# Optimization experiments

Hardware: AMD Instinct MI355X
Metric: run time of the kernel (lower is better)

The kernel has to match this reference:

```python
import jax, jax.numpy as jnp
import numpy as np

NUM_NODES = 19
INPUT_DIM = 100
HIDDEN = 128
SEQ_LEN = 250
BATCH = 64
NUM_CLASSES = 4


def setup_inputs() -> dict:
    key = jax.random.key(0)
    ks = jax.random.split(key, 12)
    s_in = 1.0 / np.sqrt(HIDDEN)  # PyTorch LSTM init scale
    inputs = jax.random.normal(ks[0], (BATCH, NUM_NODES, SEQ_LEN, INPUT_DIM), dtype=jnp.float32)
    seq_lengths = jax.random.randint(ks[1], (BATCH,), 1, SEQ_LEN + 1, dtype=jnp.int64)
    # Per-node LSTM weights, PyTorch gate order (i, f, g, o) stacked on first axis.
    W_ih = jax.random.uniform(ks[2], (NUM_NODES, 4 * HIDDEN, INPUT_DIM), jnp.float32, -s_in, s_in)
    W_hh = jax.random.uniform(ks[3], (NUM_NODES, 4 * HIDDEN, HIDDEN), jnp.float32, -s_in, s_in)
    b_ih = jax.random.uniform(ks[4], (NUM_NODES, 4 * HIDDEN), jnp.float32, -s_in, s_in)
    b_hh = jax.random.uniform(ks[5], (NUM_NODES, 4 * HIDDEN), jnp.float32, -s_in, s_in)
    feat = NUM_NODES * HIDDEN
    s1 = 1.0 / np.sqrt(feat)
    s2 = 1.0 / np.sqrt(128)
    W1 = jax.random.uniform(ks[6], (128, feat), jnp.float32, -s1, s1)
    b1 = jax.random.uniform(ks[7], (128,), jnp.float32, -s1, s1)
    W2 = jax.random.uniform(ks[8], (NUM_CLASSES, 128), jnp.float32, -s2, s2)
    b2 = jax.random.uniform(ks[9], (NUM_CLASSES,), jnp.float32, -s2, s2)
    return {"inputs": inputs, "seq_lengths": seq_lengths,
            "W_ih": W_ih, "W_hh": W_hh, "b_ih": b_ih, "b_hh": b_hh,
            "W1": W1, "b1": b1, "W2": W2, "b2": b2}


def _grouped_lstm_last(inputs, W_ih, W_hh, b_ih, b_hh):
    # inputs: [B, N, T, D] -> last hidden state per node, [B, N, H]
    B, N, T, D = inputs.shape
    H = W_hh.shape[-1]
    x = jnp.transpose(inputs, (2, 1, 0, 3))  # [T, N, B, D]
    # Precompute input projections for all timesteps: [T, N, B, 4H]
    xg = jnp.einsum('tnbd,ngd->tnbg', x, W_ih) + (b_ih + b_hh)[None, :, None, :]

    def step(carry, xg_t):
        h, c = carry  # [N, B, H]
        gates = xg_t + jnp.einsum('nbh,ngh->nbg', h, W_hh)  # [N, B, 4H]
        i, f, g, o = jnp.split(gates, 4, axis=-1)  # PyTorch gate order i,f,g,o
        i = jax.nn.sigmoid(i)
        f = jax.nn.sigmoid(f)
        g = jnp.tanh(g)
        o = jax.nn.sigmoid(o)
        c = f * c + i * g
        h = o * jnp.tanh(c)
        return (h, c), None

    h0 = jnp.zeros((N, B, H), dtype=inputs.dtype)
    (h_last, _), _ = jax.lax.scan(step, (h0, h0), xg)
    return jnp.transpose(h_last, (1, 0, 2))  # [B, N, H]


def reference(inputs, seq_lengths, W_ih, W_hh, b_ih, b_hh, W1, b1, W2, b2):
    h = _grouped_lstm_last(inputs, W_ih, W_hh, b_ih, b_hh)  # [B, N, H]
    combined = h.reshape(h.shape[0], -1)  # concat over nodes -> [B, N*H]
    hidden = jax.nn.relu(combined @ W1.T + b1)  # dropout inactive (eval)
    return hidden @ W2.T + b2  # [B, num_classes]
```

## Files before the change

### kernel.cpp

```cpp
#include <hip/hip_runtime.h>
#include <hip/hip_bf16.h>

#define NN   19
#define DIN  100
#define HID  128
#define TT   250
#define BB   64
#define NC   4
#define FEAT 2432

typedef __attribute__((ext_vector_type(8))) short s8v;
typedef __attribute__((ext_vector_type(4))) float f4v;
typedef _Float16 h8v __attribute__((ext_vector_type(8)));
typedef _Float16 h4v __attribute__((ext_vector_type(4)));

#define BFI_USH   1245184
#define V2_OFF_BFI  0ull
#define V2_OFF_BFH  2490368ull
#define V2_OFF_BIAS 4980736ull
#define V2_OFF_W1T  5019648ull
#define V2_OFF_HF   6264832ull
#define V2_NEED     6887424ull
#define PACK2_TOTAL (2*BFI_USH + 19*512 + FEAT*HID)

#define SZ_BF   (NN*8*4*8*512)
#define OFF_W1T_O (SZ_BF/2)
#define SZ_W1T  (FEAT*HID)
#define OFF_HF_O  (OFF_W1T_O + SZ_W1T)
#define PACK_TOTAL_O (SZ_BF + SZ_W1T)

__device__ __forceinline__ unsigned short f2bf(float x) {
    union { float f; unsigned u; } v; v.f = x;
    unsigned r = v.u + 0x7FFF + ((v.u >> 16) & 1);
    return (unsigned short)(r >> 16);
}
#define LOG2E 1.4426950408889634f
__device__ __forceinline__ float sigf(float x) {
    return __builtin_amdgcn_rcpf(1.f + __builtin_amdgcn_exp2f(-LOG2E * x));
}
__device__ __forceinline__ float tnhf(float x) {
    return 1.f - 2.f * __builtin_amdgcn_rcpf(__builtin_amdgcn_exp2f(2.f * LOG2E * x) + 1.f);
}

__device__ __forceinline__ void lgkm_barrier() {
    asm volatile("s_waitcnt lgkmcnt(0)" ::: "memory");
    __builtin_amdgcn_s_barrier();
    asm volatile("" ::: "memory");
}


__global__ __launch_bounds__(256) void pack2_kernel(
        const float* __restrict__ W_ih, const float* __restrict__ W_hh,
        const float* __restrict__ b_ih, const float* __restrict__ b_hh,
        const float* __restrict__ W1, char* __restrict__ wsb) {
    int id = blockIdx.x * 256 + threadIdx.x;
    if (id < 2 * BFI_USH) {
        int which = id >= BFI_USH;
        int i = which ? id - BFI_USH : id;
        int e    = i & 7;
        int lane = (i >> 3) & 63;
        int kt   = (i >> 9) & 3;
        int nt   = (i >> 11) & 3;
        int hb   = (i >> 13) & 7;
        int n    = i >> 16;
        int k = kt * 32 + (lane >> 4) * 8 + e;
        int g = nt * 128 + hb * 16 + (lane & 15);
        float v;
        if (which) v = W_hh[((size_t)n * 512 + g) * HID + k];
        else       v = (k < DIN) ? W_ih[((size_t)n * 512 + g) * DIN + k] : 0.f;
        reinterpret_cast<_Float16*>(wsb)[id] = (_Float16)v;
        return;
    }
    int id2 = id - 2 * BFI_USH;
    if (id2 < NN * 512) {
        reinterpret_cast<float*>(wsb + V2_OFF_BIAS)[id2] = b_ih[id2] + b_hh[id2];
        return;
    }
    int id3 = id2 - NN * 512;
    if (id3 < FEAT * HID) {
        int j = id3 & 127, k = id3 >> 7;
        reinterpret_cast<float*>(wsb + V2_OFF_W1T)[id3] = W1[(size_t)j * FEAT + k];
    }
}

__global__ __launch_bounds__(512, 2) void lstm8_kernel(
        const char* __restrict__ wsb, const float* __restrict__ inp,
        float* __restrict__ hf) {
    __shared__ alignas(16) _Float16 wih[8 * 16 * 512];
    __shared__ alignas(16) _Float16 xh[2][16 * 256];

    const int tid  = threadIdx.x;
    const int lane = tid & 63;
    const int w8   = tid >> 6;
    const int l15  = lane & 15;
    const int g4   = lane >> 4;
    const int n    = blockIdx.x >> 3;
    const int oct  = blockIdx.x & 7;
    const int bq   = oct >> 1;
    const int hi   = oct & 1;
    const int hb   = w8;
    const int j    = hb * 16 + l15;

    h8v bf[4][4];
    {
        const _Float16* wp = reinterpret_cast<const _Float16*>(wsb + V2_OFF_BFH)
                             + (size_t)lane * 8;
        #pragma unroll
        for (int nt = 0; nt < 4; ++nt)
            #pragma unroll
            for (int kt = 0; kt < 4; ++kt)
                bf[nt][kt] = *reinterpret_cast<const h8v*>(
                    wp + ((size_t)((n * 8 + hb) * 16 + nt * 4 + kt)) * 512);
    }
    float bs[4];
    #pragma unroll
    for (int nt = 0; nt < 4; ++nt)
        bs[nt] = reinterpret_cast<const float*>(wsb + V2_OFF_BIAS)[n * 512 + nt * 128 + j];

    {
        const h8v* src = reinterpret_cast<const h8v*>(
            reinterpret_cast<const _Float16*>(wsb + V2_OFF_BFI) + (size_t)n * 65536);
        h8v* dst = reinterpret_cast<h8v*>(wih);
        for (int i = tid; i < 8192; i += 512) dst[i] = src[i];
    }
    for (int i = tid; i < 2 * 16 * 256; i += 512) (&xh[0][0])[i] = (_Float16)0.f;

    const bool st = tid < 200;
    const int sr  = st ? tid / 25 : 0;
    const int c4  = st ? tid - sr * 25 : 0;
    const int g4s = sr >> 1, qs = sr & 1;
    const int tr  = g4s * 4 + qs;
    const int Rr  = (g4s & 1) * 4 + (g4s >> 1) * 2 + qs;
    const float* xb = inp + (size_t)((bq * 16 + hi * 8 + Rr) * NN + n) * (TT * DIN)
                      + c4 * 4;
    const int wofs_x = tr * 512 + ((c4 * 8) ^ ((tr & 7) << 4));

    const int arow = l15 * 512;
    const int aswz = (l15 & 7) << 4;
    const int wr0 = (g4 * 4) * 512 + ((256 + 2 * j) ^ (((g4 * 4) & 7) << 4));
    const int wr1 = (g4 * 4 + 1) * 512 + ((256 + 2 * j) ^ (((g4 * 4 + 1) & 7) << 4));
    const char* wfb = reinterpret_cast<const char*>(wih) + hb * 16384 + lane * 16;

    float c2[2] = {0.f, 0.f};
    float h2[2] = {0.f, 0.f};

    __syncthreads();
    if (st) {
        float4 v = *reinterpret_cast<const float4*>(xb);
        h4v pk = {(_Float16)v.x, (_Float16)v.y, (_Float16)v.z, (_Float16)v.w};
        *reinterpret_cast<h4v*>(reinterpret_cast<char*>(xh[0]) + wofs_x) = pk;
    }
    __syncthreads();

    #pragma unroll 2
    for (int t = 0; t < TT; ++t) {
        char* rc = reinterpret_cast<char*>(xh[t & 1]);
        char* wc = reinterpret_cast<char*>(xh[(t + 1) & 1]);

        float4 nxt = make_float4(0.f, 0.f, 0.f, 0.f);
        if (t < TT - 1 && st)
            nxt = *reinterpret_cast<const float4*>(xb + (t + 1) * DIN);

        f4v acc[4];
        #pragma unroll
        for (int nt = 0; nt < 4; ++nt)
            acc[nt] = (f4v){bs[nt], bs[nt], 0.f, 0.f};

        h8v ax0 = *reinterpret_cast<const h8v*>(rc + arow + ((0 * 64 + g4 * 16) ^ aswz));
        h8v ax1 = *reinterpret_cast<const h8v*>(rc + arow + ((1 * 64 + g4 * 16) ^ aswz));
        h8v ax2 = *reinterpret_cast<const h8v*>(rc + arow + ((2 * 64 + g4 * 16) ^ aswz));
        h8v ax3 = *reinterpret_cast<const h8v*>(rc + arow + ((3 * 64 + g4 * 16) ^ aswz));
        #pragma unroll
        for (int nt = 0; nt < 4; ++nt) {
            h8v w0 = *reinterpret_cast<const h8v*>(wfb + (nt * 4 + 0) * 1024);
            h8v w1 = *reinterpret_cast<const h8v*>(wfb + (nt * 4 + 1) * 1024);
            h8v w2 = *reinterpret_cast<const h8v*>(wfb + (nt * 4 + 2) * 1024);
            h8v w3 = *reinterpret_cast<const h8v*>(wfb + (nt * 4 + 3) * 1024);
            acc[nt] = __builtin_amdgcn_mfma_f32_16x16x32_f16(ax0, w0, acc[nt], 0, 0, 0);
            acc[nt] = __builtin_amdgcn_mfma_f32_16x16x32_f16(ax1, w1, acc[nt], 0, 0, 0);
            acc[nt] = __builtin_amdgcn_mfma_f32_16x16x32_f16(ax2, w2, acc[nt], 0, 0, 0);
            acc[nt] = __builtin_amdgcn_mfma_f32_16x16x32_f16(ax3, w3, acc[nt], 0, 0, 0);
        }

        h8v ah0 = *reinterpret_cast<const h8v*>(rc + arow + ((4 * 64 + g4 * 16) ^ aswz));
        h8v ah1 = *reinterpret_cast<const h8v*>(rc + arow + ((5 * 64 + g4 * 16) ^ aswz));
        h8v ah2 = *reinterpret_cast<const h8v*>(rc + arow + ((6 * 64 + g4 * 16) ^ aswz));
        h8v ah3 = *reinterpret_cast<const h8v*>(rc + arow + ((7 * 64 + g4 * 16) ^ aswz));

        acc[0] = __builtin_amdgcn_mfma_f32_16x16x32_f16(ah0, bf[0][0], acc[0], 0, 0, 0);
        acc[0] = __builtin_amdgcn_mfma_f32_16x16x32_f16(ah1, bf[0][1], acc[0], 0, 0, 0);
        acc[0] = __builtin_amdgcn_mfma_f32_16x16x32_f16(ah2, bf[0][2], acc[0], 0, 0, 0);
        acc[0] = __builtin_amdgcn_mfma_f32_16x16x32_f16(ah3, bf[0][3], acc[0], 0, 0, 0);
        float ii0 = sigf(acc[0][0]);
        float ii1 = sigf(acc[0][1]);

        acc[1] = __builtin_amdgcn_mfma_f32_16x16x32_f16(ah0, bf[1][0], acc[1], 0, 0, 0);
        acc[1] = __builtin_amdgcn_mfma_f32_16x16x32_f16(ah1, bf[1][1], acc[1], 0, 0, 0);
        acc[1] = __builtin_amdgcn_mfma_f32_16x16x32_f16(ah2, bf[1][2], acc[1], 0, 0, 0);
        acc[1] = __builtin_amdgcn_mfma_f32_16x16x32_f16(ah3, bf[1][3], acc[1], 0, 0, 0);
        float ff0 = sigf(acc[1][0]);
        float ff1 = sigf(acc[1][1]);

        acc[2] = __builtin_amdgcn_mfma_f32_16x16x32_f16(ah0, bf[2][0], acc[2], 0, 0, 0);
        acc[2] = __builtin_amdgcn_mfma_f32_16x16x32_f16(ah1, bf[2][1], acc[2], 0, 0, 0);
        acc[2] = __builtin_amdgcn_mfma_f32_16x16x32_f16(ah2, bf[2][2], acc[2], 0, 0, 0);
        acc[2] = __builtin_amdgcn_mfma_f32_16x16x32_f16(ah3, bf[2][3], acc[2], 0, 0, 0);
        float gg0 = tnhf(acc[2][0]);
        float gg1 = tnhf(acc[2][1]);

        acc[3] = __builtin_amdgcn_mfma_f32_16x16x32_f16(ah0, bf[3][0], acc[3], 0, 0, 0);
        acc[3] = __builtin_amdgcn_mfma_f32_16x16x32_f16(ah1, bf[3][1], acc[3], 0, 0, 0);
        acc[3] = __builtin_amdgcn_mfma_f32_16x16x32_f16(ah2, bf[3][2], acc[3], 0, 0, 0);
        acc[3] = __builtin_amdgcn_mfma_f32_16x16x32_f16(ah3, bf[3][3], acc[3], 0, 0, 0);
        float oo0 = sigf(acc[3][0]);
        float oo1 = sigf(acc[3][1]);

        float cn0 = ff0 * c2[0] + ii0 * gg0;
        c2[0] = cn0;
        float hn0 = oo0 * tnhf(cn0);
        h2[0] = hn0;
        *reinterpret_cast<_Float16*>(wc + wr0) = (_Float16)hn0;

        float cn1 = ff1 * c2[1] + ii1 * gg1;
        c2[1] = cn1;
        float hn1 = oo1 * tnhf(cn1);
        h2[1] = hn1;
        *reinterpret_cast<_Float16*>(wc + wr1) = (_Float16)hn1;

        if (t < TT - 1 && st) {
            h4v pk = {(_Float16)nxt.x, (_Float16)nxt.y, (_Float16)nxt.z, (_Float16)nxt.w};
            *reinterpret_cast<h4v*>(wc + wofs_x) = pk;
        }
        lgkm_barrier();
    }

    #pragma unroll
    for (int q = 0; q < 2; ++q) {
        int b = bq * 16 + hi * 8 + (g4 & 1) * 4 + (g4 >> 1) * 2 + q;
        hf[((size_t)b * NN + n) * HID + j] = h2[q];
    }
}

__global__ __launch_bounds__(256) void head2_kernel(
        const float* __restrict__ hf, const float* __restrict__ w1t,
        const float* __restrict__ b1, const float* __restrict__ W2,
        const float* __restrict__ b2, float* __restrict__ out) {
    __shared__ float comb[FEAT];
    __shared__ float par[2][HID];
    __shared__ float hid[HID];
    const int b = blockIdx.x;
    const int u  = threadIdx.x & 127;
    const int kk = threadIdx.x >> 7;
    const float* hfp = hf + (size_t)b * FEAT;
    for (int i = threadIdx.x; i < FEAT; i += 256) comb[i] = hfp[i];
    __syncthreads();

    const int k0 = kk * (FEAT / 2);
    float acc = 0.f;
    #pragma unroll 8
    for (int k = 0; k < FEAT / 2; ++k)
        acc = fmaf(comb[k0 + k], w1t[(size_t)(k0 + k) * HID + u], acc);
    par[kk][u] = acc;
    __syncthreads();
    if (kk == 0) hid[u] = fmaxf(par[0][u] + par[1][u] + b1[u], 0.f);
    __syncthreads();

    if (threadIdx.x < NC) {
        int cls = threadIdx.x;
        float a = b2[cls];
        #pragma unroll 4
        for (int k = 0; k < HID; ++k)
            a = fmaf(hid[k], W2[cls * HID + k], a);
        out[b * NC + cls] = a;
    }
}

__global__ __launch_bounds__(256) void packfb_kernel(
        const float* __restrict__ W_ih, const float* __restrict__ W_hh,
        const float* __restrict__ W1,
        unsigned short* __restrict__ bfw, float* __restrict__ w1t) {
    int id = blockIdx.x * 256 + threadIdx.x;
    if (id < SZ_BF) {
        int e    = id & 7;
        int lane = (id >> 3) & 63;
        int kt   = (id >> 9) & 7;
        int nt   = (id >> 12) & 3;
        int hb   = (id >> 14) & 7;
        int n    = id >> 17;
        int k = kt * 32 + (lane >> 4) * 8 + e;
        int g = nt * 128 + hb * 16 + (lane & 15);
        float v = 0.f;
        if (k < DIN)       v = W_ih[((size_t)n * 512 + g) * DIN + k];
        else if (k < 228)  v = W_hh[((size_t)n * 512 + g) * HID + (k - DIN)];
        bfw[id] = f2bf(v);
        return;
    }
    int id3 = id - SZ_BF;
    if (id3 < SZ_W1T) {
        int j = id3 & 127, k = id3 >> 7;
        w1t[id3] = W1[(size_t)j * FEAT + k];
    }
}

__global__ __launch_bounds__(512, 2) void lstmfb_kernel(
        const float* __restrict__ inp,
        const float* __restrict__ b_ih, const float* __restrict__ b_hh,
        const unsigned short* __restrict__ bfw, float* __restrict__ hf) {
    __shared__ alignas(16) unsigned short xh[2][16 * 256];
    const int tid  = threadIdx.x;
    const int lane = tid & 63;
    const int w    = tid >> 6;
    const int l15  = lane & 15;
    const int g4   = lane >> 4;
    const int n    = blockIdx.x >> 2;
    const int bq   = blockIdx.x & 3;
    const int j    = w * 16 + l15;

    s8v bf[4][8];
    const unsigned short* wp = bfw + ((size_t)(n * 8 + w) * 32) * 512 + lane * 8;
    #pragma unroll
    for (int nt = 0; nt < 4; ++nt)
        #pragma unroll
        for (int kt = 0; kt < 8; ++kt)
            bf[nt][kt] = *reinterpret_cast<const s8v*>(wp + (nt * 8 + kt) * 512);

    float bs[4];
    #pragma unroll
    for (int nt = 0; nt < 4; ++nt)
        bs[nt] = b_ih[n * 512 + nt * 128 + j] + b_hh[n * 512 + nt * 128 + j];

    float c[4] = {0.f, 0.f, 0.f, 0.f};
    float h[4] = {0.f, 0.f, 0.f, 0.f};
    for (int i = tid; i < 2 * 16 * 256; i += 512) (&xh[0][0])[i] = 0;

    const bool st = tid < 400;
    const int row = st ? tid / 25 : 0;
    const int c4  = st ? tid - row * 25 : 0;
    const float* xb = inp + ((size_t)(bq * 16 + row) * NN + n) * (TT * DIN) + c4 * 4;
    const int wofs = row * 512 + ((c4 * 8) ^ ((row & 7) << 4));
    const int arow = l15 * 512;
    const int aswz = (l15 & 7) << 4;

    __syncthreads();
    if (st) {
        float4 v = *reinterpret_cast<const float4*>(xb);
        unsigned lo = f2bf(v.x) | ((unsigned)f2bf(v.y) << 16);
        unsigned hi = f2bf(v.z) | ((unsigned)f2bf(v.w) << 16);
        *reinterpret_cast<uint2*>(reinterpret_cast<char*>(xh[0]) + wofs) =
            make_uint2(lo, hi);
    }
    __syncthreads();

    for (int t = 0; t < TT; ++t) {
        char* rc = reinterpret_cast<char*>(xh[t & 1]);
        char* wc = reinterpret_cast<char*>(xh[(t + 1) & 1]);
        float4 nxt = make_float4(0.f, 0.f, 0.f, 0.f);
        if (t < TT - 1 && st)
            nxt = *reinterpret_cast<const float4*>(xb + (t + 1) * DIN);

        f4v acc[4];
        #pragma unroll
        for (int nt = 0; nt < 4; ++nt)
            acc[nt] = (f4v){bs[nt], bs[nt], bs[nt], bs[nt]};
        #pragma unroll
        for (int kt = 0; kt < 8; ++kt) {
            s8v a = *reinterpret_cast<const s8v*>(rc + arow + ((kt * 64 + g4 * 16) ^ aswz));
            #pragma unroll
            for (int nt = 0; nt < 4; ++nt)
                acc[nt] = __builtin_amdgcn_mfma_f32_16x16x32_bf16(a, bf[nt][kt], acc[nt], 0, 0, 0);
        }
        #pragma unroll
        for (int r = 0; r < 4; ++r) {
            float ii = sigf(acc[0][r]);
            float ff = sigf(acc[1][r]);
            float gg = tnhf(acc[2][r]);
            float oo = sigf(acc[3][r]);
            float cn = ff * c[r] + ii * gg;
            c[r] = cn;
            float hn = oo * tnhf(cn);
            h[r] = hn;
            int rr = g4 * 4 + r;
            *reinterpret_cast<unsigned short*>(
                wc + rr * 512 + (((DIN + j) * 2) ^ ((rr & 7) << 4))) = f2bf(hn);
        }
        if (t < TT - 1 && st) {
            unsigned lo = f2bf(nxt.x) | ((unsigned)f2bf(nxt.y) << 16);
            unsigned hi = f2bf(nxt.z) | ((unsigned)f2bf(nxt.w) << 16);
            *reinterpret_cast<uint2*>(wc + wofs) = make_uint2(lo, hi);
        }
        __syncthreads();
    }
    #pragma unroll
    for (int r = 0; r < 4; ++r) {
        int b = bq * 16 + g4 * 4 + r;
        hf[((size_t)b * NN + n) * HID + j] = h[r];
    }
}

extern "C" void kernel_launch(void* const* d_in, const int* in_sizes, int n_in,
                              void* d_out, int out_size, void* d_ws, size_t ws_size,
                              hipStream_t stream) {
    const float* inp  = (const float*)d_in[0];
    const float* W_ih = (const float*)d_in[2];
    const float* W_hh = (const float*)d_in[3];
    const float* b_ih = (const float*)d_in[4];
    const float* b_hh = (const float*)d_in[5];
    const float* W1   = (const float*)d_in[6];
    const float* b1   = (const float*)d_in[7];
    const float* W2   = (const float*)d_in[8];
    const float* b2   = (const float*)d_in[9];
    float* out = (float*)d_out;

    if (ws_size >= V2_NEED) {
        char* wsb = (char*)d_ws;
        float* hf  = (float*)(wsb + V2_OFF_HF);
        float* w1t = (float*)(wsb + V2_OFF_W1T);
        pack2_kernel<<<(PACK2_TOTAL + 255) / 256, 256, 0, stream>>>(
            W_ih, W_hh, b_ih, b_hh, W1, wsb);
        lstm8_kernel<<<NN * 8, 512, 0, stream>>>(wsb, inp, hf);
        head2_kernel<<<BB, 256, 0, stream>>>(hf, w1t, b1, W2, b2, out);
    } else {
        float* ws = (float*)d_ws;
        unsigned short* bfw = (unsigned short*)d_ws;
        packfb_kernel<<<(PACK_TOTAL_O + 255) / 256, 256, 0, stream>>>(
            W_ih, W_hh, W1, bfw, ws + OFF_W1T_O);
        lstmfb_kernel<<<NN * 4, 512, 0, stream>>>(inp, b_ih, b_hh, bfw, ws + OFF_HF_O);
        head2_kernel<<<BB, 256, 0, stream>>>(ws + OFF_HF_O, ws + OFF_W1T_O,
                                             b1, W2, b2, out);
    }
}
```

Measured before the change: 333.5 us.

## Software-pipeline input projection one step ahead of the recurrent matmul

```diff
diff --git a/kernel.cpp b/kernel.cpp
--- a/kernel.cpp
+++ b/kernel.cpp
@@ -83,11 +83,12 @@
     }
 }
 
-__global__ __launch_bounds__(512, 2) void lstm8_kernel(
+__global__ __launch_bounds__(512, 2) void lstm9_kernel(
         const char* __restrict__ wsb, const float* __restrict__ inp,
         float* __restrict__ hf) {
     __shared__ alignas(16) _Float16 wih[8 * 16 * 512];
-    __shared__ alignas(16) _Float16 xh[2][16 * 256];
+    __shared__ alignas(16) _Float16 xbuf[2][16 * 128];
+    __shared__ alignas(16) _Float16 hbuf[2][16 * 128];
 
     const int tid  = threadIdx.x;
     const int lane = tid & 63;
@@ -123,7 +124,13 @@
         h8v* dst = reinterpret_cast<h8v*>(wih);
         for (int i = tid; i < 8192; i += 512) dst[i] = src[i];
     }
-    for (int i = tid; i < 2 * 16 * 256; i += 512) (&xh[0][0])[i] = (_Float16)0.f;
+    for (int i = tid; i < 2 * 16 * 128; i += 512) {
+        xbuf[0][i & 2047] = (_Float16)0.f;
+    }
+    for (int i = tid; i < 16 * 128; i += 512) {
+        xbuf[0][i] = (_Float16)0.f; xbuf[1][i] = (_Float16)0.f;
+        hbuf[0][i] = (_Float16)0.f; hbuf[1][i] = (_Float16)0.f;
+    }
 
     const bool st = tid < 200;
     const int sr  = st ? tid / 25 : 0;
@@ -133,12 +140,12 @@
     const int Rr  = (g4s & 1) * 4 + (g4s >> 1) * 2 + qs;
     const float* xb = inp + (size_t)((bq * 16 + hi * 8 + Rr) * NN + n) * (TT * DIN)
                       + c4 * 4;
-    const int wofs_x = tr * 512 + ((c4 * 8) ^ ((tr & 7) << 4));
-
-    const int arow = l15 * 512;
+    const int wofs_x = tr * 256 + ((c4 * 8) ^ ((tr & 7) << 4));
+
+    const int arow = l15 * 256;
     const int aswz = (l15 & 7) << 4;
-    const int wr0 = (g4 * 4) * 512 + ((256 + 2 * j) ^ (((g4 * 4) & 7) << 4));
-    const int wr1 = (g4 * 4 + 1) * 512 + ((256 + 2 * j) ^ (((g4 * 4 + 1) & 7) << 4));
+    const int wr0 = (g4 * 4) * 256 + ((2 * j) ^ (((g4 * 4) & 7) << 4));
+    const int wr1 = (g4 * 4 + 1) * 256 + ((2 * j) ^ (((g4 * 4 + 1) & 7) << 4));
     const char* wfb = reinterpret_cast<const char*>(wih) + hb * 16384 + lane * 16;
 
     float c2[2] = {0.f, 0.f};
@@ -146,91 +153,123 @@
 
     __syncthreads();
     if (st) {
-        float4 v = *reinterpret_cast<const float4*>(xb);
-        h4v pk = {(_Float16)v.x, (_Float16)v.y, (_Float16)v.z, (_Float16)v.w};
-        *reinterpret_cast<h4v*>(reinterpret_cast<char*>(xh[0]) + wofs_x) = pk;
-    }
-    __syncthreads();
-
-    #pragma unroll 2
-    for (int t = 0; t < TT; ++t) {
-        char* rc = reinterpret_cast<char*>(xh[t & 1]);
-        char* wc = reinterpret_cast<char*>(xh[(t + 1) & 1]);
-
-        float4 nxt = make_float4(0.f, 0.f, 0.f, 0.f);
-        if (t < TT - 1 && st)
-            nxt = *reinterpret_cast<const float4*>(xb + (t + 1) * DIN);
-
-        f4v acc[4];
-        #pragma unroll
-        for (int nt = 0; nt < 4; ++nt)
-            acc[nt] = (f4v){bs[nt], bs[nt], 0.f, 0.f};
-
-        h8v ax0 = *reinterpret_cast<const h8v*>(rc + arow + ((0 * 64 + g4 * 16) ^ aswz));
-        h8v ax1 = *reinterpret_cast<const h8v*>(rc + arow + ((1 * 64 + g4 * 16) ^ aswz));
-        h8v ax2 = *reinterpret_cast<const h8v*>(rc + arow + ((2 * 64 + g4 * 16) ^ aswz));
-        h8v ax3 = *reinterpret_cast<const h8v*>(rc + arow + ((3 * 64 + g4 * 16) ^ aswz));
+        float4 v0 = *reinterpret_cast<const float4*>(xb);
+        float4 v1 = *reinterpret_cast<const float4*>(xb + DIN);
+        h4v p0 = {(_Float16)v0.x, (_Float16)v0.y, (_Float16)v0.z, (_Float16)v0.w};
+        h4v p1 = {(_Float16)v1.x, (_Float16)v1.y, (_Float16)v1.z, (_Float16)v1.w};
+        *reinterpret_cast<h4v*>(reinterpret_cast<char*>(xbuf[0]) + wofs_x) = p0;
+        *reinterpret_cast<h4v*>(reinterpret_cast<char*>(xbuf[1]) + wofs_x) = p1;
+    }
+    __syncthreads();
+
+    f4v accC[4];
+    #pragma unroll
+    for (int nt = 0; nt < 4; ++nt)
+        accC[nt] = (f4v){bs[nt], bs[nt], 0.f, 0.f};
+    {
+        const char* rcX = reinterpret_cast<const char*>(xbuf[0]);
+        h8v ax0 = *reinterpret_cast<const h8v*>(rcX + arow + ((0 * 64 + g4 * 16) ^ aswz));
+        h8v ax1 = *reinterpret_cast<const h8v*>(rcX + arow + ((1 * 64 + g4 * 16) ^ aswz));
+        h8v ax2 = *reinterpret_cast<const h8v*>(rcX + arow + ((2 * 64 + g4 * 16) ^ aswz));
+        h8v ax3 = *reinterpret_cast<const h8v*>(rcX + arow + ((3 * 64 + g4 * 16) ^ aswz));
         #pragma unroll
         for (int nt = 0; nt < 4; ++nt) {
             h8v w0 = *reinterpret_cast<const h8v*>(wfb + (nt * 4 + 0) * 1024);
             h8v w1 = *reinterpret_cast<const h8v*>(wfb + (nt * 4 + 1) * 1024);
             h8v w2 = *reinterpret_cast<const h8v*>(wfb + (nt * 4 + 2) * 1024);
             h8v w3 = *reinterpret_cast<const h8v*>(wfb + (nt * 4 + 3) * 1024);
-            acc[nt] = __builtin_amdgcn_mfma_f32_16x16x32_f16(ax0, w0, acc[nt], 0, 0, 0);
-            acc[nt] = __builtin_amdgcn_mfma_f32_16x16x32_f16(ax1, w1, acc[nt], 0, 0, 0);
-            acc[nt] = __builtin_amdgcn_mfma_f32_16x16x32_f16(ax2, w2, acc[nt], 0, 0, 0);
-            acc[nt] = __builtin_amdgcn_mfma_f32_16x16x32_f16(ax3, w3, acc[nt], 0, 0, 0);
-        }
-
-        h8v ah0 = *reinterpret_cast<const h8v*>(rc + arow + ((4 * 64 + g4 * 16) ^ aswz));
-        h8v ah1 = *reinterpret_cast<const h8v*>(rc + arow + ((5 * 64 + g4 * 16) ^ aswz));
-        h8v ah2 = *reinterpret_cast<const h8v*>(rc + arow + ((6 * 64 + g4 * 16) ^ aswz));
-        h8v ah3 = *reinterpret_cast<const h8v*>(rc + arow + ((7 * 64 + g4 * 16) ^ aswz));
-
-        acc[0] = __builtin_amdgcn_mfma_f32_16x16x32_f16(ah0, bf[0][0], acc[0], 0, 0, 0);
-        acc[0] = __builtin_amdgcn_mfma_f32_16x16x32_f16(ah1, bf[0][1], acc[0], 0, 0, 0);
-        acc[0] = __builtin_amdgcn_mfma_f32_16x16x32_f16(ah2, bf[0][2], acc[0], 0, 0, 0);
-        acc[0] = __builtin_amdgcn_mfma_f32_16x16x32_f16(ah3, bf[0][3], acc[0], 0, 0, 0);
-        float ii0 = sigf(acc[0][0]);
-        float ii1 = sigf(acc[0][1]);
-
-        acc[1] = __builtin_amdgcn_mfma_f32_16x16x32_f16(ah0, bf[1][0], acc[1], 0, 0, 0);
-        acc[1] = __builtin_amdgcn_mfma_f32_16x16x32_f16(ah1, bf[1][1], acc[1], 0, 0, 0);
-        acc[1] = __builtin_amdgcn_mfma_f32_16x16x32_f16(ah2, bf[1][2], acc[1], 0, 0, 0);
-        acc[1] = __builtin_amdgcn_mfma_f32_16x16x32_f16(ah3, bf[1][3], acc[1], 0, 0, 0);
-        float ff0 = sigf(acc[1][0]);
-        float ff1 = sigf(acc[1][1]);
-
-        acc[2] = __builtin_amdgcn_mfma_f32_16x16x32_f16(ah0, bf[2][0], acc[2], 0, 0, 0);
-        acc[2] = __builtin_amdgcn_mfma_f32_16x16x32_f16(ah1, bf[2][1], acc[2], 0, 0, 0);
-        acc[2] = __builtin_amdgcn_mfma_f32_16x16x32_f16(ah2, bf[2][2], acc[2], 0, 0, 0);
-        acc[2] = __builtin_amdgcn_mfma_f32_16x16x32_f16(ah3, bf[2][3], acc[2], 0, 0, 0);
-        float gg0 = tnhf(acc[2][0]);
-        float gg1 = tnhf(acc[2][1]);
-
-        acc[3] = __builtin_amdgcn_mfma_f32_16x16x32_f16(ah0, bf[3][0], acc[3], 0, 0, 0);
-        acc[3] = __builtin_amdgcn_mfma_f32_16x16x32_f16(ah1, bf[3][1], acc[3], 0, 0, 0);
-        acc[3] = __builtin_amdgcn_mfma_f32_16x16x32_f16(ah2, bf[3][2], acc[3], 0, 0, 0);
-        acc[3] = __builtin_amdgcn_mfma_f32_16x16x32_f16(ah3, bf[3][3], acc[3], 0, 0, 0);
-        float oo0 = sigf(acc[3][0]);
-        float oo1 = sigf(acc[3][1]);
+            accC[nt] = __builtin_amdgcn_mfma_f32_16x16x32_f16(ax0, w0, accC[nt], 0, 0, 0);
+            accC[nt] = __builtin_amdgcn_mfma_f32_16x16x32_f16(ax1, w1, accC[nt], 0, 0, 0);
+            accC[nt] = __builtin_amdgcn_mfma_f32_16x16x32_f16(ax2, w2, accC[nt], 0, 0, 0);
+            accC[nt] = __builtin_amdgcn_mfma_f32_16x16x32_f16(ax3, w3, accC[nt], 0, 0, 0);
+        }
+    }
+    lgkm_barrier();
+
+    #pragma unroll 2
+    for (int t = 0; t < TT; ++t) {
+        const char* rcH = reinterpret_cast<const char*>(hbuf[t & 1]);
+        char*       wcH = reinterpret_cast<char*>(hbuf[(t + 1) & 1]);
+        char*       wcX = reinterpret_cast<char*>(xbuf[t & 1]);
+        const char* rcX = reinterpret_cast<const char*>(xbuf[(t + 1) & 1]);
+
+        float4 nxt = make_float4(0.f, 0.f, 0.f, 0.f);
+        int t2 = t + 2 < TT ? t + 2 : TT - 1;
+        if (st) nxt = *reinterpret_cast<const float4*>(xb + (size_t)t2 * DIN);
+
+        h8v ah0 = *reinterpret_cast<const h8v*>(rcH + arow + ((0 * 64 + g4 * 16) ^ aswz));
+        h8v ah1 = *reinterpret_cast<const h8v*>(rcH + arow + ((1 * 64 + g4 * 16) ^ aswz));
+        h8v ah2 = *reinterpret_cast<const h8v*>(rcH + arow + ((2 * 64 + g4 * 16) ^ aswz));
+        h8v ah3 = *reinterpret_cast<const h8v*>(rcH + arow + ((3 * 64 + g4 * 16) ^ aswz));
+
+        accC[0] = __builtin_amdgcn_mfma_f32_16x16x32_f16(ah0, bf[0][0], accC[0], 0, 0, 0);
+        accC[0] = __builtin_amdgcn_mfma_f32_16x16x32_f16(ah1, bf[0][1], accC[0], 0, 0, 0);
+        accC[0] = __builtin_amdgcn_mfma_f32_16x16x32_f16(ah2, bf[0][2], accC[0], 0, 0, 0);
+        accC[0] = __builtin_amdgcn_mfma_f32_16x16x32_f16(ah3, bf[0][3], accC[0], 0, 0, 0);
+        float ii0 = sigf(accC[0][0]);
+        float ii1 = sigf(accC[0][1]);
+
+        accC[1] = __builtin_amdgcn_mfma_f32_16x16x32_f16(ah0, bf[1][0], accC[1], 0, 0, 0);
+        accC[1] = __builtin_amdgcn_mfma_f32_16x16x32_f16(ah1, bf[1][1], accC[1], 0, 0, 0);
+        accC[1] = __builtin_amdgcn_mfma_f32_16x16x32_f16(ah2, bf[1][2], accC[1], 0, 0, 0);
+        accC[1] = __builtin_amdgcn_mfma_f32_16x16x32_f16(ah3, bf[1][3], accC[1], 0, 0, 0);
+        float ff0 = sigf(accC[1][0]);
+        float ff1 = sigf(accC[1][1]);
+
+        accC[2] = __builtin_amdgcn_mfma_f32_16x16x32_f16(ah0, bf[2][0], accC[2], 0, 0, 0);
+        accC[2] = __builtin_amdgcn_mfma_f32_16x16x32_f16(ah1, bf[2][1], accC[2], 0, 0, 0);
+        accC[2] = __builtin_amdgcn_mfma_f32_16x16x32_f16(ah2, bf[2][2], accC[2], 0, 0, 0);
+        accC[2] = __builtin_amdgcn_mfma_f32_16x16x32_f16(ah3, bf[2][3], accC[2], 0, 0, 0);
+        float gg0 = tnhf(accC[2][0]);
+        float gg1 = tnhf(accC[2][1]);
+
+        accC[3] = __builtin_amdgcn_mfma_f32_16x16x32_f16(ah0, bf[3][0], accC[3], 0, 0, 0);
+        accC[3] = __builtin_amdgcn_mfma_f32_16x16x32_f16(ah1, bf[3][1], accC[3], 0, 0, 0);
+        accC[3] = __builtin_amdgcn_mfma_f32_16x16x32_f16(ah2, bf[3][2], accC[3], 0, 0, 0);
+        accC[3] = __builtin_amdgcn_mfma_f32_16x16x32_f16(ah3, bf[3][3], accC[3], 0, 0, 0);
+        float oo0 = sigf(accC[3][0]);
+        float oo1 = sigf(accC[3][1]);
 
         float cn0 = ff0 * c2[0] + ii0 * gg0;
         c2[0] = cn0;
         float hn0 = oo0 * tnhf(cn0);
         h2[0] = hn0;
-        *reinterpret_cast<_Float16*>(wc + wr0) = (_Float16)hn0;
+        *reinterpret_cast<_Float16*>(wcH + wr0) = (_Float16)hn0;
 
         float cn1 = ff1 * c2[1] + ii1 * gg1;
         c2[1] = cn1;
         float hn1 = oo1 * tnhf(cn1);
         h2[1] = hn1;
-        *reinterpret_cast<_Float16*>(wc + wr1) = (_Float16)hn1;
-
-        if (t < TT - 1 && st) {
+        *reinterpret_cast<_Float16*>(wcH + wr1) = (_Float16)hn1;
+
+        if (st) {
             h4v pk = {(_Float16)nxt.x, (_Float16)nxt.y, (_Float16)nxt.z, (_Float16)nxt.w};
-            *reinterpret_cast<h4v*>(wc + wofs_x) = pk;
-        }
+            *reinterpret_cast<h4v*>(wcX + wofs_x) = pk;
+        }
+
+        f4v accN[4];
+        #pragma unroll
+        for (int nt = 0; nt < 4; ++nt)
+            accN[nt] = (f4v){bs[nt], bs[nt], 0.f, 0.f};
+
+        h8v ax0 = *reinterpret_cast<const h8v*>(rcX + arow + ((0 * 64 + g4 * 16) ^ aswz));
+        h8v ax1 = *reinterpret_cast<const h8v*>(rcX + arow + ((1 * 64 + g4 * 16) ^ aswz));
+        h8v ax2 = *reinterpret_cast<const h8v*>(rcX + arow + ((2 * 64 + g4 * 16) ^ aswz));
+        h8v ax3 = *reinterpret_cast<const h8v*>(rcX + arow + ((3 * 64 + g4 * 16) ^ aswz));
+        #pragma unroll
+        for (int nt = 0; nt < 4; ++nt) {
+            h8v w0 = *reinterpret_cast<const h8v*>(wfb + (nt * 4 + 0) * 1024);
+            h8v w1 = *reinterpret_cast<const h8v*>(wfb + (nt * 4 + 1) * 1024);
+            h8v w2 = *reinterpret_cast<const h8v*>(wfb + (nt * 4 + 2) * 1024);
+            h8v w3 = *reinterpret_cast<const h8v*>(wfb + (nt * 4 + 3) * 1024);
+            accN[nt] = __builtin_amdgcn_mfma_f32_16x16x32_f16(ax0, w0, accN[nt], 0, 0, 0);
+            accN[nt] = __builtin_amdgcn_mfma_f32_16x16x32_f16(ax1, w1, accN[nt], 0, 0, 0);
+            accN[nt] = __builtin_amdgcn_mfma_f32_16x16x32_f16(ax2, w2, accN[nt], 0, 0, 0);
+            accN[nt] = __builtin_amdgcn_mfma_f32_16x16x32_f16(ax3, w3, accN[nt], 0, 0, 0);
+        }
+        #pragma unroll
+        for (int nt = 0; nt < 4; ++nt) accC[nt] = accN[nt];
+
         lgkm_barrier();
     }
 
@@ -417,7 +456,7 @@
         float* w1t = (float*)(wsb + V2_OFF_W1T);
         pack2_kernel<<<(PACK2_TOTAL + 255) / 256, 256, 0, stream>>>(
             W_ih, W_hh, b_ih, b_hh, W1, wsb);
-        lstm8_kernel<<<NN * 8, 512, 0, stream>>>(wsb, inp, hf);
+        lstm9_kernel<<<NN * 8, 512, 0, stream>>>(wsb, inp, hf);
         head2_kernel<<<BB, 256, 0, stream>>>(hf, w1t, b1, W2, b2, out);
     } else {
         float* ws = (float*)d_ws;
```

New measurement: 336.7 us. No clear change (+1.0%).
